# Performance work log

Measured on AMD Instinct MI355X. Metric: run time of the kernel, lower is better.

The kernel has to match this reference:

```python
import jax, jax.numpy as jnp
import numpy as np

N, E, D, H, ED = 50000, 800000, 64, 8, 16
DH = D // H  # 8


def setup_inputs() -> dict:
    key = jax.random.key(0)
    ks = jax.random.split(key, 16)
    s = 0.05
    return {
        "x": jax.random.normal(ks[0], (N, D), jnp.float32),
        "edge_index": jax.random.randint(ks[1], (2, E), 0, N, jnp.int32),
        "edge_attr": jax.random.normal(ks[2], (E, ED), jnp.float32),
        "Wq": jax.random.normal(ks[3], (D, D), jnp.float32) * s,
        "bq": jnp.zeros((D,), jnp.float32),
        "Wk": jax.random.normal(ks[4], (D, D), jnp.float32) * s,
        "bk": jnp.zeros((D,), jnp.float32),
        "Wv": jax.random.normal(ks[5], (D, D), jnp.float32) * s,
        "bv": jnp.zeros((D,), jnp.float32),
        "We": jax.random.normal(ks[6], (ED, D), jnp.float32) * s,
        "be": jnp.zeros((D,), jnp.float32),
        "Wskip": jax.random.normal(ks[7], (D, D), jnp.float32) * s,
        "bskip": jnp.zeros((D,), jnp.float32),
        "Wbeta": jax.random.normal(ks[8], (3 * D, 1), jnp.float32) * s,
        "gamma": jnp.ones((D,), jnp.float32),
        "beta_bn": jnp.zeros((D,), jnp.float32),
    }


def reference(x, edge_index, edge_attr, Wq, bq, Wk, bk, Wv, bv, We, be,
              Wskip, bskip, Wbeta, gamma, beta_bn):
    n, d = x.shape
    src, dst = edge_index[0], edge_index[1]
    # per-node projections, then gather per edge (PyG TransformerConv)
    q = (x @ Wq + bq).reshape(n, H, DH)
    k = (x @ Wk + bk).reshape(n, H, DH)
    v = (x @ Wv + bv).reshape(n, H, DH)
    e = (edge_attr @ We + be).reshape(-1, H, DH)
    ke = k[src] + e                      # [E,H,DH]
    ve = v[src] + e                      # [E,H,DH]
    logits = (q[dst] * ke).sum(-1) / jnp.sqrt(jnp.float32(DH))  # [E,H]
    # segment softmax over incoming edges of each destination node
    m = jax.ops.segment_max(logits, dst, num_segments=n)
    p = jnp.exp(logits - m[dst])
    denom = jax.ops.segment_sum(p, dst, num_segments=n)
    alpha = p / (denom[dst] + 1e-16)     # [E,H]
    out = jax.ops.segment_sum(alpha[:, :, None] * ve, dst, num_segments=n)
    out = out.reshape(n, d)              # concat heads
    # beta-gated skip connection (beta=True, root_weight=True)
    x_r = x @ Wskip + bskip
    g = jax.nn.sigmoid(jnp.concatenate([out, x_r, out - x_r], axis=-1) @ Wbeta)
    out = g * x_r + (1.0 - g) * out
    # BatchNorm1d (training forward: batch statistics), eps=1e-5
    mean = out.mean(axis=0)
    var = out.var(axis=0)
    out = (out - mean) * jax.lax.rsqrt(var + 1e-5) * gamma + beta_bn
    # LeakyReLU(0.01); dropout is identity in eval
    return jnp.where(out >= 0, out, 0.01 * out)
```

## Files before the change

kernel.cpp:

```cpp
#include <hip/hip_runtime.h>

#define D   64
#define H   8
#define DH  8
#define ED  16
#define QK_SCALE 0.35355339059327373f

typedef unsigned int uint_t;

__device__ __forceinline__ void fma4(float4& a, float s, const float4& w) {
    a.x += s * w.x; a.y += s * w.y; a.z += s * w.z; a.w += s * w.w;
}
__device__ __forceinline__ uint_t f2bf(float f) {
    uint_t u = __float_as_uint(f);
    return (u + 0x7FFFu + ((u >> 16) & 1u)) >> 16;
}
__device__ __forceinline__ float bf_lo(uint_t u) { return __uint_as_float(u << 16); }
__device__ __forceinline__ float bf_hi(uint_t u) { return __uint_as_float(u & 0xFFFF0000u); }

__global__ __launch_bounds__(256) void proj_qs_hist(
    const float* __restrict__ x,
    const float* __restrict__ Wq, const float* __restrict__ bq,
    const float* __restrict__ Ws, const float* __restrict__ bs,
    const float* __restrict__ We, const float* __restrict__ be,
    float* __restrict__ q, float* __restrict__ xr,
    uint_t* __restrict__ Ap, float* __restrict__ qbe, int N,
    const int* __restrict__ ei, int* __restrict__ cnt, int E, int projBlocks)
{
    __shared__ float sW[2][D * D];
    __shared__ float sWe[ED * D];
    __shared__ float sbe[D];
    if (blockIdx.x >= projBlocks) {
        int gid = (blockIdx.x - projBlocks) * 256 + threadIdx.x;
        if (gid < E) atomicAdd(&cnt[ei[E + gid]], 1);
        return;
    }
    {
        for (int t = threadIdx.x; t < D * D; t += 256) {
            sW[0][t] = Wq[t];
            sW[1][t] = Ws[t];
        }
        for (int t = threadIdx.x; t < ED * D; t += 256) sWe[t] = We[t];
        if (threadIdx.x < D) sbe[threadIdx.x] = be[threadIdx.x];
    }
    __syncthreads();

    int cg = (threadIdx.x & 15) * 4;
    float4 vbq = *(const float4*)(bq + cg);
    float4 vbs = *(const float4*)(bs + cg);
    int h  = cg >> 3;
    int hh = (cg >> 2) & 1;

    #pragma unroll 1
    for (int it = 0; it < 4; ++it) {
        int node = blockIdx.x * 64 + it * 16 + (threadIdx.x >> 4);
        if (node >= N) return;

        float4 aq = {0,0,0,0}, as_ = {0,0,0,0};
        const float* xrow = x + (size_t)node * D;

        #pragma unroll
        for (int i = 0; i < D; i += 4) {
            float4 xv = *(const float4*)(xrow + i);
            #pragma unroll
            for (int s = 0; s < 4; ++s) {
                float xs = (&xv.x)[s];
                fma4(aq,  xs, *(const float4*)(&sW[0][(i + s) * D + cg]));
                fma4(as_, xs, *(const float4*)(&sW[1][(i + s) * D + cg]));
            }
        }
        aq.x = (aq.x + vbq.x) * QK_SCALE;
        aq.y = (aq.y + vbq.y) * QK_SCALE;
        aq.z = (aq.z + vbq.z) * QK_SCALE;
        aq.w = (aq.w + vbq.w) * QK_SCALE;
        as_.x += vbs.x; as_.y += vbs.y; as_.z += vbs.z; as_.w += vbs.w;

        size_t o = (size_t)node * D + cg;
        *(float4*)(q  + o) = aq;
        *(float4*)(xr + o) = as_;

        float part[ED];
        #pragma unroll
        for (int i = 0; i < ED; ++i) {
            float pi = 0.f;
            #pragma unroll
            for (int s = 0; s < 4; ++s)
                pi += (&aq.x)[s] * sWe[i * D + cg + s];
            part[i] = pi;
        }
        float qb = 0.f;
        #pragma unroll
        for (int s = 0; s < 4; ++s) qb += (&aq.x)[s] * sbe[cg + s];
        #pragma unroll
        for (int i = 0; i < ED; ++i) part[i] += __shfl_xor(part[i], 1);
        qb += __shfl_xor(qb, 1);

        uint4 apk;
        apk.x = f2bf(part[hh * 8 + 0]) | (f2bf(part[hh * 8 + 1]) << 16);
        apk.y = f2bf(part[hh * 8 + 2]) | (f2bf(part[hh * 8 + 3]) << 16);
        apk.z = f2bf(part[hh * 8 + 4]) | (f2bf(part[hh * 8 + 5]) << 16);
        apk.w = f2bf(part[hh * 8 + 6]) | (f2bf(part[hh * 8 + 7]) << 16);
        *(uint4*)(Ap + (size_t)node * 64 + h * 8 + hh * 4) = apk;
        if (hh == 0) qbe[(size_t)node * 8 + h] = qb;
    }
}

__global__ __launch_bounds__(256) void proj_kv_scana(
    const float* __restrict__ x,
    const float* __restrict__ Wk, const float* __restrict__ bk,
    const float* __restrict__ Wv, const float* __restrict__ bv,
    uint_t* __restrict__ kvp, int N, int kvBlocks,
    const int* __restrict__ cnt, int* __restrict__ bsum)
{
    __shared__ float sW[2][D * D];
    __shared__ int red[256];
    if (blockIdx.x >= kvBlocks) {
        int t = threadIdx.x;
        int i = (blockIdx.x - kvBlocks) * 256 + t;
        red[t] = (i < N) ? cnt[i] : 0;
        __syncthreads();
        for (int s = 128; s > 0; s >>= 1) {
            if (t < s) red[t] += red[t + s];
            __syncthreads();
        }
        if (t == 0) bsum[blockIdx.x - kvBlocks] = red[0];
        return;
    }
    for (int t = threadIdx.x; t < D * D; t += 256) {
        sW[0][t] = Wk[t];
        sW[1][t] = Wv[t];
    }
    __syncthreads();

    int cg = (threadIdx.x & 15) * 4;
    float4 vbk = *(const float4*)(bk + cg);
    float4 vbv = *(const float4*)(bv + cg);

    #pragma unroll 1
    for (int it = 0; it < 4; ++it) {
        int node = blockIdx.x * 64 + it * 16 + (threadIdx.x >> 4);
        if (node >= N) return;

        float4 ak = {0,0,0,0}, av = {0,0,0,0};
        const float* xrow = x + (size_t)node * D;

        #pragma unroll
        for (int i = 0; i < D; i += 4) {
            float4 xv = *(const float4*)(xrow + i);
            #pragma unroll
            for (int s = 0; s < 4; ++s) {
                float xs = (&xv.x)[s];
                fma4(ak, xs, *(const float4*)(&sW[0][(i + s) * D + cg]));
                fma4(av, xs, *(const float4*)(&sW[1][(i + s) * D + cg]));
            }
        }
        ak.x += vbk.x; ak.y += vbk.y; ak.z += vbk.z; ak.w += vbk.w;
        av.x += vbv.x; av.y += vbv.y; av.z += vbv.z; av.w += vbv.w;

        uint4 pkv;
        pkv.x = f2bf(ak.x) | (f2bf(av.x) << 16);
        pkv.y = f2bf(ak.y) | (f2bf(av.y) << 16);
        pkv.z = f2bf(ak.z) | (f2bf(av.z) << 16);
        pkv.w = f2bf(ak.w) | (f2bf(av.w) << 16);
        *(uint4*)(kvp + (size_t)node * D + cg) = pkv;
    }
}

__global__ __launch_bounds__(256) void scan_b(int* __restrict__ bsum, int nb)
{
    __shared__ int sh[256];
    int t = threadIdx.x;
    int v = (t < nb) ? bsum[t] : 0;
    sh[t] = v;
    __syncthreads();
    for (int s = 1; s < 256; s <<= 1) {
        int a = (t >= s) ? sh[t - s] : 0;
        __syncthreads();
        sh[t] += a;
        __syncthreads();
    }
    if (t < nb) bsum[t] = sh[t] - v;
}

__global__ __launch_bounds__(256) void scan_c(
    const int* __restrict__ cnt, const int* __restrict__ bsum,
    int* __restrict__ row_start, int* __restrict__ cursor, int N, int E)
{
    __shared__ int sh[256];
    int t = threadIdx.x;
    int i = blockIdx.x * 256 + t;
    int v = (i < N) ? cnt[i] : 0;
    sh[t] = v;
    __syncthreads();
    for (int s = 1; s < 256; s <<= 1) {
        int a = (t >= s) ? sh[t - s] : 0;
        __syncthreads();
        sh[t] += a;
        __syncthreads();
    }
    int excl = sh[t] - v + bsum[blockIdx.x];
    if (i < N) { row_start[i] = excl; cursor[i] = excl; }
    if (i == N - 1) row_start[N] = E;
}

__global__ __launch_bounds__(256) void csr_scatter(
    const int* __restrict__ ei, const float4* __restrict__ ea4,
    int* __restrict__ cursor, int* __restrict__ srcs_s,
    uint_t* __restrict__ ea_s, int E)
{
    int gid = blockIdx.x * 256 + threadIdx.x;
    if (gid >= E) return;
    int src = ei[gid];
    int dst = ei[E + gid];
    float4 r0 = ea4[(size_t)gid * 4 + 0];
    float4 r1 = ea4[(size_t)gid * 4 + 1];
    float4 r2 = ea4[(size_t)gid * 4 + 2];
    float4 r3 = ea4[(size_t)gid * 4 + 3];
    int pos = atomicAdd(&cursor[dst], 1);
    srcs_s[pos] = src;
    uint4 p0, p1;
    p0.x = f2bf(r0.x) | (f2bf(r0.y) << 16);
    p0.y = f2bf(r0.z) | (f2bf(r0.w) << 16);
    p0.z = f2bf(r1.x) | (f2bf(r1.y) << 16);
    p0.w = f2bf(r1.z) | (f2bf(r1.w) << 16);
    p1.x = f2bf(r2.x) | (f2bf(r2.y) << 16);
    p1.y = f2bf(r2.z) | (f2bf(r2.w) << 16);
    p1.z = f2bf(r3.x) | (f2bf(r3.y) << 16);
    p1.w = f2bf(r3.z) | (f2bf(r3.w) << 16);
    *(uint4*)(ea_s + (size_t)pos * 8)     = p0;
    *(uint4*)(ea_s + (size_t)pos * 8 + 4) = p1;
}

__global__ __launch_bounds__(256) void node_gather(
    const int*   __restrict__ row_start,
    const int*   __restrict__ srcs_s,
    const uint_t* __restrict__ ea_s,
    const float* __restrict__ We, const float* __restrict__ be,
    const float* __restrict__ q, const uint_t* __restrict__ kvp,
    const float* __restrict__ xr,
    const uint_t* __restrict__ Ap, const float* __restrict__ qbe,
    const float* __restrict__ Wbeta,
    float* __restrict__ out, float* __restrict__ S1p, float* __restrict__ S2p,
    int N)
{
    __shared__ float l1[4][D];
    __shared__ float l2[4][D];
    int lane = threadIdx.x & 63;
    int w    = threadIdx.x >> 6;
    int t    = lane & 7;

    float rWe[ED];
    #pragma unroll
    for (int i = 0; i < ED; ++i) rWe[i] = We[i * D + lane];
    float bev = be[lane];
    float wb0 = Wbeta[lane], wb1 = Wbeta[D + lane], wb2 = Wbeta[2 * D + lane];

    float s1bn = 0.f, s2bn = 0.f;
    int stride = gridDim.x * 4;

    for (int nid = blockIdx.x * 4 + w; nid < N; nid += stride) {
        int rs  = row_start[nid];
        int deg = row_start[nid + 1] - rs;

        float  qv   = q[(size_t)nid * D + lane];
        uint_t au   = Ap[(size_t)nid * 64 + lane];
        float  a0   = bf_lo(au), a1 = bf_hi(au);
        float  qbeh = qbe[(size_t)nid * 8 + (lane >> 3)];

        float acc = 0.f, den = 0.f, s0 = 0.f, s1 = 0.f;

        int srcv = 0;
        if (lane < deg) srcv = srcs_s[rs + lane];

        int nb = (deg < 64) ? deg : 64;
        for (int j0 = 0; j0 < nb; j0 += 4) {
            int m = nb - j0; if (m > 4) m = 4;
            uint_t eald = ea_s[(size_t)(rs + j0) * 8 + (lane & 31)];
            uint_t kvu[4];
            #pragma unroll
            for (int j = 0; j < 4; ++j) {
                int jj = (j < m) ? (j0 + j) : j0;
                int s  = __builtin_amdgcn_readlane(srcv, jj);
                kvu[j] = kvp[(size_t)s * D + lane];
            }
            #pragma unroll
            for (int j = 0; j < 4; ++j) {
                if (j < m) {
                    uint_t eau = __shfl(eald, j * 8 + t);
                    float kf = bf_lo(kvu[j]), vf = bf_hi(kvu[j]);
                    float ex = bf_lo(eau), ey = bf_hi(eau);
                    float c = qv * kf + ex * a0 + ey * a1;
                    c += __shfl_xor(c, 1);
                    c += __shfl_xor(c, 2);
                    c += __shfl_xor(c, 4);
                    float p = __expf(c + qbeh);
                    acc += p * vf;
                    den += p;
                    s0  += p * ex;
                    s1  += p * ey;
                }
            }
        }
        for (int j = 64; j < deg; ++j) {
            int s = srcs_s[rs + j];
            uint_t kvu = kvp[(size_t)s * D + lane];
            uint_t eau = ea_s[(size_t)(rs + j) * 8 + t];
            float kf = bf_lo(kvu), vf = bf_hi(kvu);
            float ex = bf_lo(eau), ey = bf_hi(eau);
            float c = qv * kf + ex * a0 + ey * a1;
            c += __shfl_xor(c, 1);
            c += __shfl_xor(c, 2);
            c += __shfl_xor(c, 4);
            float p = __expf(c + qbeh);
            acc += p * vf; den += p;
            s0 += p * ex; s1 += p * ey;
        }

        float esum = 0.f;
        #pragma unroll
        for (int i = 0; i < ED; ++i) {
            int srcl = (lane & 56) + (i >> 1);
            float sv = (i & 1) ? __shfl(s1, srcl) : __shfl(s0, srcl);
            esum += sv * rWe[i];
        }

        float o   = (acc + esum + bev * den) / (den + 1e-16f);
        float xrv = xr[(size_t)nid * D + lane];
        float tb  = o * wb0 + xrv * wb1 + (o - xrv) * wb2;
        #pragma unroll
        for (int s = 1; s < 64; s <<= 1) tb += __shfl_xor(tb, s);
        float g  = 1.f / (1.f + __expf(-tb));
        float o2 = g * xrv + (1.f - g) * o;
        out[(size_t)nid * D + lane] = o2;
        s1bn += o2; s2bn += o2 * o2;
    }

    l1[w][lane] = s1bn; l2[w][lane] = s2bn;
    __syncthreads();
    if (threadIdx.x < D) {
        float a = l1[0][threadIdx.x] + l1[1][threadIdx.x]
                + l1[2][threadIdx.x] + l1[3][threadIdx.x];
        float b = l2[0][threadIdx.x] + l2[1][threadIdx.x]
                + l2[2][threadIdx.x] + l2[3][threadIdx.x];
        unsafeAtomicAdd(&S1p[threadIdx.x * 64], a);
        unsafeAtomicAdd(&S2p[threadIdx.x * 64], b);
    }
}

__global__ __launch_bounds__(256) void bn_apply(
    float4* __restrict__ out, const float* __restrict__ S1p,
    const float* __restrict__ S2p, const float* __restrict__ gamma,
    const float* __restrict__ beta, int total4, float invN)
{
    int gid = blockIdx.x * 256 + threadIdx.x;
    if (gid >= total4) return;
    int col = (gid & 15) * 4;
    float4 g4 = *(const float4*)(gamma + col);
    float4 b4 = *(const float4*)(beta + col);
    float4 y  = out[gid];
    #pragma unroll
    for (int j = 0; j < 4; ++j) {
        float mean = S1p[(col + j) * 64] * invN;
        float var  = S2p[(col + j) * 64] * invN - mean * mean;
        float sc   = (&g4.x)[j] * rsqrtf(var + 1e-5f);
        float sh   = (&b4.x)[j] - mean * sc;
        float tv   = (&y.x)[j] * sc + sh;
        (&y.x)[j]  = (tv >= 0.f) ? tv : 0.01f * tv;
    }
    out[gid] = y;
}

extern "C" void kernel_launch(void* const* d_in, const int* in_sizes, int n_in,
                              void* d_out, int out_size, void* d_ws, size_t ws_size,
                              hipStream_t stream)
{
    const float* x     = (const float*)d_in[0];
    const int*   ei    = (const int*)  d_in[1];
    const float* ea    = (const float*)d_in[2];
    const float* Wq    = (const float*)d_in[3];
    const float* bq    = (const float*)d_in[4];
    const float* Wk    = (const float*)d_in[5];
    const float* bk    = (const float*)d_in[6];
    const float* Wv    = (const float*)d_in[7];
    const float* bv    = (const float*)d_in[8];
    const float* We    = (const float*)d_in[9];
    const float* be    = (const float*)d_in[10];
    const float* Wskip = (const float*)d_in[11];
    const float* bskip = (const float*)d_in[12];
    const float* Wbeta = (const float*)d_in[13];
    const float* gamma = (const float*)d_in[14];
    const float* betab = (const float*)d_in[15];

    int N = in_sizes[0] / D;
    int E = in_sizes[1] / 2;

    int*    ws        = (int*)d_ws;
    int*    cnt       = ws;
    float*  S1p       = (float*)(ws + 50000);
    float*  S2p       = (float*)(ws + 54096);
    int*    row_start = ws + 58192;
    int*    bsum      = ws + 108240;
    int*    srcs_s    = ws + 108544;
    uint_t* ea_s      = (uint_t*)(ws + 908544);
    uint_t* kvp       = (uint_t*)(ws + 7308544);
    float*  q         = (float*)(ws + 10508544);
    float*  xr        = (float*)(ws + 13708544);
    uint_t* Ap        = (uint_t*)(ws + 16908544);
    float*  qbe       = (float*)(ws + 20108544);

    hipMemsetAsync(d_ws, 0, (size_t)58192 * sizeof(int), stream);

    int projB = (N + 63) / 64;
    int histB = (E + 255) / 256;
    proj_qs_hist<<<projB + histB, 256, 0, stream>>>(
        x, Wq, bq, Wskip, bskip, We, be,
        q, xr, Ap, qbe, N, ei, cnt, E, projB);

    int scanB = (N + 255) / 256;
    proj_kv_scana<<<projB + scanB, 256, 0, stream>>>(
        x, Wk, bk, Wv, bv, kvp, N, projB, cnt, bsum);

    scan_b<<<1, 256, 0, stream>>>(bsum, scanB);
    scan_c<<<scanB, 256, 0, stream>>>(cnt, bsum, row_start, cnt, N, E);

    csr_scatter<<<(E + 255) / 256, 256, 0, stream>>>(
        ei, (const float4*)ea, cnt, srcs_s, ea_s, E);

    node_gather<<<1024, 256, 0, stream>>>(
        row_start, srcs_s, ea_s, We, be, q, kvp, xr, Ap, qbe, Wbeta,
        (float*)d_out, S1p, S2p, N);

    bn_apply<<<(N * 16 + 255) / 256, 256, 0, stream>>>(
        (float4*)d_out, S1p, S2p, gamma, betab, N * 16, 1.0f / (float)N);
}
```

Baseline: 226.3 us.

## Remap node_gather lanes to head×edge so each lane processes a whole head per edge

Changes the node_gather work mapping: instead of each lane owning one feature channel and iterating edges with shuffle reductions per edge, each lane now owns one head and one of eight concurrent edges. Each lane loads a full 16-byte key/value and edge-attr vector and computes the head dot product locally. Partial sums are reduced across edge groups with xor shuffles at the end, and results are permuted back to channel layout. This removes per-edge cross-lane reductions and processes eight edges per iteration, at the cost of many more registers (acc, sv and ex arrays) and a 4-blocks-per-CU launch bound that may force spills.

```diff
diff --git a/kernel.cpp b/kernel.cpp
--- a/kernel.cpp
+++ b/kernel.cpp
@@ -231,7 +231,7 @@
     *(uint4*)(ea_s + (size_t)pos * 8 + 4) = p1;
 }
 
-__global__ __launch_bounds__(256) void node_gather(
+__global__ __launch_bounds__(256, 4) void node_gather(
     const int*   __restrict__ row_start,
     const int*   __restrict__ srcs_s,
     const uint_t* __restrict__ ea_s,
@@ -247,12 +247,15 @@
     __shared__ float l2[4][D];
     int lane = threadIdx.x & 63;
     int w    = threadIdx.x >> 6;
-    int t    = lane & 7;
+    int h    = lane & 7;
+    int e    = lane >> 3;
+    int cmix = h * 8 + e;
+    int perm = (h << 3) | e;
 
     float rWe[ED];
     #pragma unroll
-    for (int i = 0; i < ED; ++i) rWe[i] = We[i * D + lane];
-    float bev = be[lane];
+    for (int i = 0; i < ED; ++i) rWe[i] = We[i * D + cmix];
+    float bev = be[cmix];
     float wb0 = Wbeta[lane], wb1 = Wbeta[D + lane], wb2 = Wbeta[2 * D + lane];
 
     float s1bn = 0.f, s2bn = 0.f;
@@ -262,69 +265,80 @@
         int rs  = row_start[nid];
         int deg = row_start[nid + 1] - rs;
 
-        float  qv   = q[(size_t)nid * D + lane];
-        uint_t au   = Ap[(size_t)nid * 64 + lane];
-        float  a0   = bf_lo(au), a1 = bf_hi(au);
-        float  qbeh = qbe[(size_t)nid * 8 + (lane >> 3)];
-
-        float acc = 0.f, den = 0.f, s0 = 0.f, s1 = 0.f;
-
-        int srcv = 0;
-        if (lane < deg) srcv = srcs_s[rs + lane];
-
-        int nb = (deg < 64) ? deg : 64;
-        for (int j0 = 0; j0 < nb; j0 += 4) {
-            int m = nb - j0; if (m > 4) m = 4;
-            uint_t eald = ea_s[(size_t)(rs + j0) * 8 + (lane & 31)];
-            uint_t kvu[4];
+        const float* qp = q + (size_t)nid * D + h * 8;
+        float4 q0 = *(const float4*)qp;
+        float4 q1 = *(const float4*)(qp + 4);
+        const uint4* app = (const uint4*)(Ap + (size_t)nid * 64 + h * 8);
+        uint4 au0 = app[0], au1 = app[1];
+        float a16[ED];
+        #pragma unroll
+        for (int j = 0; j < 4; ++j) {
+            a16[(j & 3) * 2]     = bf_lo((&au0.x)[j]);
+            a16[(j & 3) * 2 + 1] = bf_hi((&au0.x)[j]);
+            a16[8 + (j & 3) * 2]     = bf_lo((&au1.x)[j]);
+            a16[8 + (j & 3) * 2 + 1] = bf_hi((&au1.x)[j]);
+        }
+        float qbeh = qbe[(size_t)nid * 8 + h];
+
+        float acc[8] = {0,0,0,0,0,0,0,0};
+        float sv[ED] = {0,0,0,0,0,0,0,0,0,0,0,0,0,0,0,0};
+        float den = 0.f;
+
+        for (int j0 = 0; j0 < deg; j0 += 8) {
+            int eidx = j0 + e;
+            bool valid = eidx < deg;
+            int ce = valid ? eidx : 0;
+            int src = srcs_s[rs + ce];
+
+            const uint4* kp = (const uint4*)(kvp + (size_t)src * 64 + h * 8);
+            uint4 k0 = kp[0], k1 = kp[1];
+            const uint4* ep = (const uint4*)(ea_s + (size_t)(rs + ce) * 8);
+            uint4 e0 = ep[0], e1 = ep[1];
+
+            float ex[ED];
             #pragma unroll
             for (int j = 0; j < 4; ++j) {
-                int jj = (j < m) ? (j0 + j) : j0;
-                int s  = __builtin_amdgcn_readlane(srcv, jj);
-                kvu[j] = kvp[(size_t)s * D + lane];
+                ex[j * 2]         = bf_lo((&e0.x)[j]);
+                ex[j * 2 + 1]     = bf_hi((&e0.x)[j]);
+                ex[8 + j * 2]     = bf_lo((&e1.x)[j]);
+                ex[8 + j * 2 + 1] = bf_hi((&e1.x)[j]);
             }
-            #pragma unroll
-            for (int j = 0; j < 4; ++j) {
-                if (j < m) {
-                    uint_t eau = __shfl(eald, j * 8 + t);
-                    float kf = bf_lo(kvu[j]), vf = bf_hi(kvu[j]);
-                    float ex = bf_lo(eau), ey = bf_hi(eau);
-                    float c = qv * kf + ex * a0 + ey * a1;
-                    c += __shfl_xor(c, 1);
-                    c += __shfl_xor(c, 2);
-                    c += __shfl_xor(c, 4);
-                    float p = __expf(c + qbeh);
-                    acc += p * vf;
-                    den += p;
-                    s0  += p * ex;
-                    s1  += p * ey;
-                }
-            }
-        }
-        for (int j = 64; j < deg; ++j) {
-            int s = srcs_s[rs + j];
-            uint_t kvu = kvp[(size_t)s * D + lane];
-            uint_t eau = ea_s[(size_t)(rs + j) * 8 + t];
-            float kf = bf_lo(kvu), vf = bf_hi(kvu);
-            float ex = bf_lo(eau), ey = bf_hi(eau);
-            float c = qv * kf + ex * a0 + ey * a1;
-            c += __shfl_xor(c, 1);
-            c += __shfl_xor(c, 2);
-            c += __shfl_xor(c, 4);
-            float p = __expf(c + qbeh);
-            acc += p * vf; den += p;
-            s0 += p * ex; s1 += p * ey;
-        }
-
+            float c = qbeh;
+            c += (&q0.x)[0] * bf_lo(k0.x); c += (&q0.x)[1] * bf_lo(k0.y);
+            c += (&q0.x)[2] * bf_lo(k0.z); c += (&q0.x)[3] * bf_lo(k0.w);
+            c += (&q1.x)[0] * bf_lo(k1.x); c += (&q1.x)[1] * bf_lo(k1.y);
+            c += (&q1.x)[2] * bf_lo(k1.z); c += (&q1.x)[3] * bf_lo(k1.w);
+            #pragma unroll
+            for (int i = 0; i < ED; ++i) c += ex[i] * a16[i];
+
+            float p = valid ? __expf(c) : 0.f;
+            den += p;
+            acc[0] += p * bf_hi(k0.x); acc[1] += p * bf_hi(k0.y);
+            acc[2] += p * bf_hi(k0.z); acc[3] += p * bf_hi(k0.w);
+            acc[4] += p * bf_hi(k1.x); acc[5] += p * bf_hi(k1.y);
+            acc[6] += p * bf_hi(k1.z); acc[7] += p * bf_hi(k1.w);
+            #pragma unroll
+            for (int i = 0; i < ED; ++i) sv[i] += p * ex[i];
+        }
+
+        #pragma unroll
+        for (int m = 8; m <= 32; m <<= 1) {
+            den += __shfl_xor(den, m);
+            #pragma unroll
+            for (int i = 0; i < 8; ++i) acc[i] += __shfl_xor(acc[i], m);
+            #pragma unroll
+            for (int i = 0; i < ED; ++i) sv[i] += __shfl_xor(sv[i], m);
+        }
+        float vsum = acc[0];
+        #pragma unroll
+        for (int i = 1; i < 8; ++i) vsum = (e == i) ? acc[i] : vsum;
         float esum = 0.f;
         #pragma unroll
-        for (int i = 0; i < ED; ++i) {
-            int srcl = (lane & 56) + (i >> 1);
-            float sv = (i & 1) ? __shfl(s1, srcl) : __shfl(s0, srcl);
-            esum += sv * rWe[i];
-        }
-
-        float o   = (acc + esum + bev * den) / (den + 1e-16f);
+        for (int i = 0; i < ED; ++i) esum += rWe[i] * sv[i];
+
+        float o_mix = (vsum + esum + bev * den) / (den + 1e-16f);
+        float o = __shfl(o_mix, perm);
+
         float xrv = xr[(size_t)nid * D + lane];
         float tb  = o * wb0 + xrv * wb1 + (o - xrv) * wb2;
         #pragma unroll
```

Measured after the change: 217.6 us. -3.8%, faster.

## Remap node_gather to edge-parallel lanes over two nodes; fuse block-sum scan into scan_c

Applied to the files above, without the earlier changes.

Each wave now handles two destination nodes at once, and its 64 lanes are split into 8 heads × 8 edge slots. Each lane gathers full 8-wide k/v and edge-attribute vectors for one edge, and results are combined with cross-lane reductions (khreduce8 and xor shuffles) at the end. This replaces the per-edge serial loop and its per-edge shuffle reductions, aiming for more memory-level parallelism. The cost is higher register pressure (launch bounds set to 3 waves) and extra reduction work when degrees are low. Separately, the single-block scan_b kernel is removed: every scan_c block now redundantly scans the block sums itself, saving one launch.

```diff
diff --git a/kernel.cpp b/kernel.cpp
--- a/kernel.cpp
+++ b/kernel.cpp
@@ -17,6 +17,27 @@
 }
 __device__ __forceinline__ float bf_lo(uint_t u) { return __uint_as_float(u << 16); }
 __device__ __forceinline__ float bf_hi(uint_t u) { return __uint_as_float(u & 0xFFFF0000u); }
+
+__device__ __forceinline__ float khreduce8(const float* acc, int e) {
+    int b0 = e & 1, b1 = (e >> 1) & 1, b2 = (e >> 2) & 1;
+    float t0[4];
+    #pragma unroll
+    for (int j = 0; j < 4; ++j) {
+        float k = b0 ? acc[2*j+1] : acc[2*j];
+        float s = b0 ? acc[2*j]   : acc[2*j+1];
+        t0[j] = k + __shfl_xor(s, 8);
+    }
+    float t1[2];
+    #pragma unroll
+    for (int j = 0; j < 2; ++j) {
+        float k = b1 ? t0[2*j+1] : t0[2*j];
+        float s = b1 ? t0[2*j]   : t0[2*j+1];
+        t1[j] = k + __shfl_xor(s, 16);
+    }
+    float k = b2 ? t1[1] : t1[0];
+    float s = b2 ? t1[0] : t1[1];
+    return k + __shfl_xor(s, 32);
+}
 
 __global__ __launch_bounds__(256) void proj_qs_hist(
     const float* __restrict__ x,
@@ -166,28 +187,24 @@
     }
 }
 
-__global__ __launch_bounds__(256) void scan_b(int* __restrict__ bsum, int nb)
-{
+__global__ __launch_bounds__(256) void scan_c(
+    const int* __restrict__ cnt, const int* __restrict__ bsum,
+    int* __restrict__ row_start, int* __restrict__ cursor, int N, int E, int nb)
+{
+    __shared__ int sb[256];
     __shared__ int sh[256];
     int t = threadIdx.x;
-    int v = (t < nb) ? bsum[t] : 0;
-    sh[t] = v;
+    int bv = (t < nb) ? bsum[t] : 0;
+    sb[t] = bv;
     __syncthreads();
     for (int s = 1; s < 256; s <<= 1) {
-        int a = (t >= s) ? sh[t - s] : 0;
+        int a = (t >= s) ? sb[t - s] : 0;
         __syncthreads();
-        sh[t] += a;
+        sb[t] += a;
         __syncthreads();
     }
-    if (t < nb) bsum[t] = sh[t] - v;
-}
-
-__global__ __launch_bounds__(256) void scan_c(
-    const int* __restrict__ cnt, const int* __restrict__ bsum,
-    int* __restrict__ row_start, int* __restrict__ cursor, int N, int E)
-{
-    __shared__ int sh[256];
-    int t = threadIdx.x;
+    int boff = sb[blockIdx.x] - bsum[blockIdx.x];
+
     int i = blockIdx.x * 256 + t;
     int v = (i < N) ? cnt[i] : 0;
     sh[t] = v;
@@ -198,7 +215,7 @@
         sh[t] += a;
         __syncthreads();
     }
-    int excl = sh[t] - v + bsum[blockIdx.x];
+    int excl = sh[t] - v + boff;
     if (i < N) { row_start[i] = excl; cursor[i] = excl; }
     if (i == N - 1) row_start[N] = E;
 }
@@ -231,7 +248,43 @@
     *(uint4*)(ea_s + (size_t)pos * 8 + 4) = p1;
 }
 
-__global__ __launch_bounds__(256) void node_gather(
+#define GBODY(rs_, deg_, qa_, qb_, aA_, aB_, qbe_, acc_, sv_, den_)            \
+{                                                                              \
+    int eidx = j0 + e;                                                         \
+    bool valid = eidx < (deg_);                                                \
+    int ce = valid ? eidx : 0;                                                 \
+    int src = srcs_s[(rs_) + ce];                                              \
+    const uint4* kp = (const uint4*)(kvp + (size_t)src * 64 + h * 8);          \
+    uint4 k0 = kp[0], k1 = kp[1];                                              \
+    const uint4* ep = (const uint4*)(ea_s + (size_t)((rs_) + ce) * 8);         \
+    uint4 u0 = ep[0], u1 = ep[1];                                              \
+    float c = qbe_;                                                            \
+    c += qa_.x * bf_lo(k0.x) + qa_.y * bf_lo(k0.y)                             \
+       + qa_.z * bf_lo(k0.z) + qa_.w * bf_lo(k0.w);                            \
+    c += qb_.x * bf_lo(k1.x) + qb_.y * bf_lo(k1.y)                             \
+       + qb_.z * bf_lo(k1.z) + qb_.w * bf_lo(k1.w);                            \
+    float ex[ED];                                                              \
+    ex[0]=bf_lo(u0.x); ex[1]=bf_hi(u0.x); ex[2]=bf_lo(u0.y); ex[3]=bf_hi(u0.y);\
+    ex[4]=bf_lo(u0.z); ex[5]=bf_hi(u0.z); ex[6]=bf_lo(u0.w); ex[7]=bf_hi(u0.w);\
+    ex[8]=bf_lo(u1.x); ex[9]=bf_hi(u1.x); ex[10]=bf_lo(u1.y);ex[11]=bf_hi(u1.y);\
+    ex[12]=bf_lo(u1.z);ex[13]=bf_hi(u1.z);ex[14]=bf_lo(u1.w);ex[15]=bf_hi(u1.w);\
+    c += ex[0]*bf_lo(aA_.x) + ex[1]*bf_hi(aA_.x) + ex[2]*bf_lo(aA_.y)          \
+       + ex[3]*bf_hi(aA_.y) + ex[4]*bf_lo(aA_.z) + ex[5]*bf_hi(aA_.z)          \
+       + ex[6]*bf_lo(aA_.w) + ex[7]*bf_hi(aA_.w);                              \
+    c += ex[8]*bf_lo(aB_.x) + ex[9]*bf_hi(aB_.x) + ex[10]*bf_lo(aB_.y)         \
+       + ex[11]*bf_hi(aB_.y) + ex[12]*bf_lo(aB_.z) + ex[13]*bf_hi(aB_.z)       \
+       + ex[14]*bf_lo(aB_.w) + ex[15]*bf_hi(aB_.w);                            \
+    float p = valid ? __expf(c) : 0.f;                                         \
+    den_ += p;                                                                 \
+    acc_[0]+=p*bf_hi(k0.x); acc_[1]+=p*bf_hi(k0.y);                            \
+    acc_[2]+=p*bf_hi(k0.z); acc_[3]+=p*bf_hi(k0.w);                            \
+    acc_[4]+=p*bf_hi(k1.x); acc_[5]+=p*bf_hi(k1.y);                            \
+    acc_[6]+=p*bf_hi(k1.z); acc_[7]+=p*bf_hi(k1.w);                            \
+    _Pragma("unroll")                                                          \
+    for (int i = 0; i < ED; ++i) sv_[i] += p * ex[i];                          \
+}
+
+__global__ __launch_bounds__(256, 3) void node_gather(
     const int*   __restrict__ row_start,
     const int*   __restrict__ srcs_s,
     const uint_t* __restrict__ ea_s,
@@ -247,95 +300,99 @@
     __shared__ float l2[4][D];
     int lane = threadIdx.x & 63;
     int w    = threadIdx.x >> 6;
-    int t    = lane & 7;
+    int h    = lane & 7;
+    int e    = lane >> 3;
+    int cmix = h * 8 + e;
 
     float rWe[ED];
     #pragma unroll
-    for (int i = 0; i < ED; ++i) rWe[i] = We[i * D + lane];
-    float bev = be[lane];
-    float wb0 = Wbeta[lane], wb1 = Wbeta[D + lane], wb2 = Wbeta[2 * D + lane];
+    for (int i = 0; i < ED; ++i) rWe[i] = We[i * D + cmix];
+    float bev = be[cmix];
+    float wb0 = Wbeta[cmix], wb1 = Wbeta[D + cmix], wb2 = Wbeta[2 * D + cmix];
 
     float s1bn = 0.f, s2bn = 0.f;
-    int stride = gridDim.x * 4;
-
-    for (int nid = blockIdx.x * 4 + w; nid < N; nid += stride) {
-        int rs  = row_start[nid];
-        int deg = row_start[nid + 1] - rs;
-
-        float  qv   = q[(size_t)nid * D + lane];
-        uint_t au   = Ap[(size_t)nid * 64 + lane];
-        float  a0   = bf_lo(au), a1 = bf_hi(au);
-        float  qbeh = qbe[(size_t)nid * 8 + (lane >> 3)];
-
-        float acc = 0.f, den = 0.f, s0 = 0.f, s1 = 0.f;
-
-        int srcv = 0;
-        if (lane < deg) srcv = srcs_s[rs + lane];
-
-        int nb = (deg < 64) ? deg : 64;
-        for (int j0 = 0; j0 < nb; j0 += 4) {
-            int m = nb - j0; if (m > 4) m = 4;
-            uint_t eald = ea_s[(size_t)(rs + j0) * 8 + (lane & 31)];
-            uint_t kvu[4];
+    int stride  = gridDim.x * 4;
+    int stride2 = stride * 2;
+
+    for (int n0 = blockIdx.x * 4 + w; n0 < N; n0 += stride2) {
+        int n1   = n0 + stride;
+        bool has1 = n1 < N;
+        int n1c  = has1 ? n1 : n0;
+
+        int rs0 = row_start[n0], deg0 = row_start[n0 + 1] - rs0;
+        int rs1 = row_start[n1c];
+        int deg1 = has1 ? (row_start[n1c + 1] - rs1) : 0;
+
+        const float* qp0 = q + (size_t)n0 * D + h * 8;
+        float4 qa0 = *(const float4*)qp0, qb0 = *(const float4*)(qp0 + 4);
+        const float* qp1 = q + (size_t)n1c * D + h * 8;
+        float4 qa1 = *(const float4*)qp1, qb1 = *(const float4*)(qp1 + 4);
+
+        const uint4* ap0 = (const uint4*)(Ap + (size_t)n0 * 64 + h * 8);
+        uint4 aA0 = ap0[0], aB0 = ap0[1];
+        const uint4* ap1 = (const uint4*)(Ap + (size_t)n1c * 64 + h * 8);
+        uint4 aA1 = ap1[0], aB1 = ap1[1];
+
+        float qbe0 = qbe[(size_t)n0 * 8 + h];
+        float qbe1 = qbe[(size_t)n1c * 8 + h];
+
+        float acc0[8] = {0,0,0,0,0,0,0,0};
+        float acc1[8] = {0,0,0,0,0,0,0,0};
+        float sv0[ED] = {0,0,0,0,0,0,0,0,0,0,0,0,0,0,0,0};
+        float sv1[ED] = {0,0,0,0,0,0,0,0,0,0,0,0,0,0,0,0};
+        float den0 = 0.f, den1 = 0.f;
+
+        int nbmax = deg0 > deg1 ? deg0 : deg1;
+        for (int j0 = 0; j0 < nbmax; j0 += 8) {
+            if (j0 < deg0) GBODY(rs0, deg0, qa0, qb0, aA0, aB0, qbe0, acc0, sv0, den0)
+            if (j0 < deg1) GBODY(rs1, deg1, qa1, qb1, aA1, aB1, qbe1, acc1, sv1, den1)
+        }
+
+        #pragma unroll
+        for (int m = 8; m <= 32; m <<= 1) {
+            den0 += __shfl_xor(den0, m);
+            den1 += __shfl_xor(den1, m);
             #pragma unroll
-            for (int j = 0; j < 4; ++j) {
-                int jj = (j < m) ? (j0 + j) : j0;
-                int s  = __builtin_amdgcn_readlane(srcv, jj);
-                kvu[j] = kvp[(size_t)s * D + lane];
+            for (int i = 0; i < ED; ++i) {
+                sv0[i] += __shfl_xor(sv0[i], m);
+                sv1[i] += __shfl_xor(sv1[i], m);
             }
-            #pragma unroll
-            for (int j = 0; j < 4; ++j) {
-                if (j < m) {
-                    uint_t eau = __shfl(eald, j * 8 + t);
-                    float kf = bf_lo(kvu[j]), vf = bf_hi(kvu[j]);
-                    float ex = bf_lo(eau), ey = bf_hi(eau);
-                    float c = qv * kf + ex * a0 + ey * a1;
-                    c += __shfl_xor(c, 1);
-                    c += __shfl_xor(c, 2);
-                    c += __shfl_xor(c, 4);
-                    float p = __expf(c + qbeh);
-                    acc += p * vf;
-                    den += p;
-                    s0  += p * ex;
-                    s1  += p * ey;
-                }
-            }
-        }
-        for (int j = 64; j < deg; ++j) {
-            int s = srcs_s[rs + j];
-            uint_t kvu = kvp[(size_t)s * D + lane];
-            uint_t eau = ea_s[(size_t)(rs + j) * 8 + t];
-            float kf = bf_lo(kvu), vf = bf_hi(kvu);
-            float ex = bf_lo(eau), ey = bf_hi(eau);
-            float c = qv * kf + ex * a0 + ey * a1;
-            c += __shfl_xor(c, 1);
-            c += __shfl_xor(c, 2);
-            c += __shfl_xor(c, 4);
-            float p = __expf(c + qbeh);
-            acc += p * vf; den += p;
-            s0 += p * ex; s1 += p * ey;
-        }
-
-        float esum = 0.f;
+        }
+        float vs0 = khreduce8(acc0, e);
+        float vs1 = khreduce8(acc1, e);
+
+        float es0 = 0.f, es1 = 0.f;
         #pragma unroll
         for (int i = 0; i < ED; ++i) {
-            int srcl = (lane & 56) + (i >> 1);
-            float sv = (i & 1) ? __shfl(s1, srcl) : __shfl(s0, srcl);
-            esum += sv * rWe[i];
-        }
-
-        float o   = (acc + esum + bev * den) / (den + 1e-16f);
-        float xrv = xr[(size_t)nid * D + lane];
-        float tb  = o * wb0 + xrv * wb1 + (o - xrv) * wb2;
-        #pragma unroll
-        for (int s = 1; s < 64; s <<= 1) tb += __shfl_xor(tb, s);
-        float g  = 1.f / (1.f + __expf(-tb));
-        float o2 = g * xrv + (1.f - g) * o;
-        out[(size_t)nid * D + lane] = o2;
-        s1bn += o2; s2bn += o2 * o2;
-    }
-
-    l1[w][lane] = s1bn; l2[w][lane] = s2bn;
+            es0 += rWe[i] * sv0[i];
+            es1 += rWe[i] * sv1[i];
+        }
+
+        float o0 = (vs0 + es0 + bev * den0) / (den0 + 1e-16f);
+        float o1 = (vs1 + es1 + bev * den1) / (den1 + 1e-16f);
+
+        float xr0 = xr[(size_t)n0 * D + cmix];
+        float xr1 = xr[(size_t)n1c * D + cmix];
+        float tb0 = o0 * wb0 + xr0 * wb1 + (o0 - xr0) * wb2;
+        float tb1 = o1 * wb0 + xr1 * wb1 + (o1 - xr1) * wb2;
+        #pragma unroll
+        for (int s = 1; s < 64; s <<= 1) {
+            tb0 += __shfl_xor(tb0, s);
+            tb1 += __shfl_xor(tb1, s);
+        }
+        float g0 = 1.f / (1.f + __expf(-tb0));
+        float o20 = g0 * xr0 + (1.f - g0) * o0;
+        out[(size_t)n0 * D + cmix] = o20;
+        s1bn += o20; s2bn += o20 * o20;
+        if (has1) {
+            float g1 = 1.f / (1.f + __expf(-tb1));
+            float o21 = g1 * xr1 + (1.f - g1) * o1;
+            out[(size_t)n1 * D + cmix] = o21;
+            s1bn += o21; s2bn += o21 * o21;
+        }
+    }
+
+    l1[w][cmix] = s1bn; l2[w][cmix] = s2bn;
     __syncthreads();
     if (threadIdx.x < D) {
         float a = l1[0][threadIdx.x] + l1[1][threadIdx.x]
@@ -420,8 +477,7 @@
     proj_kv_scana<<<projB + scanB, 256, 0, stream>>>(
         x, Wk, bk, Wv, bv, kvp, N, projB, cnt, bsum);
 
-    scan_b<<<1, 256, 0, stream>>>(bsum, scanB);
-    scan_c<<<scanB, 256, 0, stream>>>(cnt, bsum, row_start, cnt, N, E);
+    scan_c<<<scanB, 256, 0, stream>>>(cnt, bsum, row_start, cnt, N, E, scanB);
 
     csr_scatter<<<(E + 255) / 256, 256, 0, stream>>>(
         ei, (const float4*)ea, cnt, srcs_s, ea_s, E);
```

Measured after the change: 252.8 us. 1.12x slower.
